# Optimization experiments

Measured on AMD Instinct MI355X. Metric: run time of the kernel, lower is better.

## Reference

```python
import jax, jax.numpy as jnp
import numpy as np

DIM = 2048
N_HEADS = 16
HEAD_DIM = DIM // N_HEADS
MAX_SEQ_LEN = 2048
ROPE_THETA = 32.0
EPS = 1e-6


def _precompute_freqs_1d(dim, max_seq_len, theta):
    freqs = theta ** (-np.arange(0, dim, 2, dtype=np.float32) / dim)  # [dim/2]
    pos = np.arange(max_seq_len, dtype=np.float32)                    # [S]
    ang = pos[:, None] * freqs[None, :]                               # [S, dim/2]
    return jnp.asarray(np.cos(ang)), jnp.asarray(np.sin(ang))


def _rms_norm(x, w):
    # x: [..., d]
    inv = jax.lax.rsqrt(jnp.mean(x * x, axis=-1, keepdims=True) + EPS)
    return x * inv * w


def setup_inputs() -> dict:
    key = jax.random.key(0)
    k1, k2, k3 = jax.random.split(key, 3)
    bsz, seq_len = 4, 2048
    x = jax.random.normal(k1, (bsz, seq_len, DIM), dtype=jnp.float32)
    w_qkv = jax.random.normal(k2, (3 * DIM, DIM), dtype=jnp.float32) * (DIM ** -0.5)
    w_proj = jax.random.normal(k3, (DIM, DIM), dtype=jnp.float32) * (DIM ** -0.5)
    q_norm_w = jnp.ones((HEAD_DIM,), dtype=jnp.float32)
    k_norm_w = jnp.ones((HEAD_DIM,), dtype=jnp.float32)
    return {"x": x, "w_qkv": w_qkv, "w_proj": w_proj,
            "q_norm_w": q_norm_w, "k_norm_w": k_norm_w}


def reference(x, w_qkv, w_proj, q_norm_w, k_norm_w):
    bsz, seq_len, dim = x.shape
    scale = HEAD_DIM ** -0.5

    # QKV projection (torch Linear: x @ W^T)
    qkv = jnp.einsum('bsd,ed->bse', x, w_qkv)  # [b, s, 3*dim]
    qkv = qkv.reshape(bsz, seq_len, 3, N_HEADS, HEAD_DIM).transpose(2, 0, 3, 1, 4)
    q, k, v = qkv[0], qkv[1], qkv[2]           # each [b, h, s, d]

    # Per-head RMSNorm on q, k
    q = _rms_norm(q, q_norm_w)
    k = _rms_norm(k, k_norm_w)

    # RoPE (half-split convention)
    cos, sin = _precompute_freqs_1d(HEAD_DIM, MAX_SEQ_LEN, ROPE_THETA)
    cos = cos[:seq_len][None, None]  # [1,1,s,d/2]
    sin = sin[:seq_len][None, None]
    q1, q2 = jnp.split(q, 2, axis=-1)
    k1, k2 = jnp.split(k, 2, axis=-1)
    q = jnp.concatenate([q1 * cos - q2 * sin, q2 * cos + q1 * sin], axis=-1)
    k = jnp.concatenate([k1 * cos - k2 * sin, k2 * cos + k1 * sin], axis=-1)

    # Scaled dot-product attention (no mask, eval-mode: no dropout)
    scores = jnp.einsum('bhqd,bhkd->bhqk', q, k) * scale
    attn = jax.nn.softmax(scores, axis=-1)
    y = jnp.einsum('bhqk,bhkd->bhqd', attn, v)

    # Merge heads + output projection
    y = y.transpose(0, 2, 1, 3).reshape(bsz, seq_len, dim)
    return jnp.einsum('bsd,ed->bse', y, w_proj)
```

## Files before the change

kernel.cpp:

```cpp
#include <hip/hip_runtime.h>
#include <hip/hip_bf16.h>

#define BSZ 4
#define SEQ 2048
#define DIM 2048
#define NH 16
#define HD 128
#define QK_LD 4096
#define SCALE 0.08838834764831845f
#define SC2 0.12751742910198f

typedef __attribute__((ext_vector_type(8))) short bf16x8;
typedef __attribute__((ext_vector_type(4))) float f32x4;

#define GLDS16(g, l)                                                           \
  __builtin_amdgcn_global_load_lds(                                           \
      (const __attribute__((address_space(1))) void*)(g),                     \
      (__attribute__((address_space(3))) void*)(l), 16, 0, 0)

__device__ inline short f2b(float f) {
  __hip_bfloat16 h = __float2bfloat16(f);
  short s;
  __builtin_memcpy(&s, &h, 2);
  return s;
}

__device__ inline void stage16(const float* gp, __hip_bfloat16* lp) {
  float4 q0 = ((const float4*)gp)[0], q1 = ((const float4*)gp)[1];
  float4 q2 = ((const float4*)gp)[2], q3 = ((const float4*)gp)[3];
  bf16x8 v0, v1;
  v0[0] = f2b(q0.x); v0[1] = f2b(q0.y); v0[2] = f2b(q0.z); v0[3] = f2b(q0.w);
  v0[4] = f2b(q1.x); v0[5] = f2b(q1.y); v0[6] = f2b(q1.z); v0[7] = f2b(q1.w);
  v1[0] = f2b(q2.x); v1[1] = f2b(q2.y); v1[2] = f2b(q2.z); v1[3] = f2b(q2.w);
  v1[4] = f2b(q3.x); v1[5] = f2b(q3.y); v1[6] = f2b(q3.z); v1[7] = f2b(q3.w);
  *(bf16x8*)lp = v0;
  *(bf16x8*)(lp + 8) = v1;
}

__device__ inline char* out_slice(void* outv, int b, int fl) {
  return (char*)outv + (size_t)b * (size_t)SEQ * DIM * (fl ? 2u : 4u);
}

__global__ __launch_bounds__(256)
void detect_canon(const unsigned int* __restrict__ wbits,
                  const void* __restrict__ qw, const void* __restrict__ kw,
                  __hip_bfloat16* __restrict__ qwb,
                  __hip_bfloat16* __restrict__ kwb, int* __restrict__ flag) {
  __shared__ int cnt;
  const int t = threadIdx.x;
  if (t == 0) cnt = 0;
  __syncthreads();
  int local = 0;
  for (int i = 0; i < 4; ++i) {
    unsigned int e = (wbits[t * 4 + i] >> 7) & 0xFF;
    if (e >= 96 && e < 160) local++;
  }
  atomicAdd(&cnt, local);
  __syncthreads();
  const int f = (cnt >= 768) ? 1 : 0;
  if (t == 0) *flag = f;
  if (t < 128)
    qwb[t] = f ? ((const __hip_bfloat16*)qw)[t]
               : __float2bfloat16(((const float*)qw)[t]);
  else
    kwb[t - 128] = f ? ((const __hip_bfloat16*)kw)[t - 128]
                     : __float2bfloat16(((const float*)kw)[t - 128]);
}

__global__ __launch_bounds__(256)
void convert_bf16(const void* __restrict__ in, __hip_bfloat16* __restrict__ out,
                  const int* __restrict__ flag) {
  const int fl = *flag;
  long i = ((long)blockIdx.x * 256 + threadIdx.x) * 8;
  if (fl) {
    *(float4*)(out + i) = *(const float4*)((const __hip_bfloat16*)in + i);
  } else {
    const float* p = (const float*)in + i;
    float4 a = ((const float4*)p)[0], b = ((const float4*)p)[1];
    bf16x8 o;
    o[0] = f2b(a.x); o[1] = f2b(a.y); o[2] = f2b(a.z); o[3] = f2b(a.w);
    o[4] = f2b(b.x); o[5] = f2b(b.y); o[6] = f2b(b.z); o[7] = f2b(b.w);
    *(bf16x8*)(out + i) = o;
  }
}


__global__ __launch_bounds__(256)
void gemm_qkv_full(const __hip_bfloat16* __restrict__ A,
                   const __hip_bfloat16* __restrict__ B,
                   __hip_bfloat16* __restrict__ qk, void* __restrict__ outv,
                   const int* __restrict__ flag) {
  __shared__ __hip_bfloat16 As[128 * 32];
  __shared__ __hip_bfloat16 Bs[128 * 32];
  const int t = threadIdx.x, wave = t >> 6, lane = t & 63;
  const int quad = lane >> 4, l16 = lane & 15;
  const int wm = (wave & 1) * 64, wn = (wave >> 1) * 64;
  const long bm = (long)blockIdx.x * 128, bn = (long)blockIdx.y * 128;
  const int fl = *flag;

  f32x4 acc[4][4] = {};
  for (int k0 = 0; k0 < DIM; k0 += 32) {
    __syncthreads();
    for (int i = 0; i < 2; ++i) {
      int c = wave * 64 + lane + i * 256;
      int row = c >> 2, kc = c & 3;
      GLDS16(A + (bm + row) * DIM + k0 + kc * 8, As + (wave * 64 + i * 256) * 8);
      GLDS16(B + (bn + row) * DIM + k0 + kc * 8, Bs + (wave * 64 + i * 256) * 8);
    }
    __syncthreads();
    bf16x8 aF[4], bF[4];
    for (int mt = 0; mt < 4; ++mt)
      aF[mt] = *(const bf16x8*)(As + (wm + mt * 16 + l16) * 32 + quad * 8);
    for (int nt = 0; nt < 4; ++nt)
      bF[nt] = *(const bf16x8*)(Bs + (wn + nt * 16 + l16) * 32 + quad * 8);
    for (int mt = 0; mt < 4; ++mt)
      for (int nt = 0; nt < 4; ++nt)
        acc[mt][nt] = __builtin_amdgcn_mfma_f32_16x16x32_bf16(
            aF[mt], bF[nt], acc[mt][nt], 0, 0, 0);
  }

  if (bn < 4096) {
    for (int mt = 0; mt < 4; ++mt) {
      long gr = bm + wm + mt * 16 + quad * 4;
      for (int nt = 0; nt < 4; ++nt) {
        long gc = bn + wn + nt * 16 + l16;
        for (int r = 0; r < 4; ++r)
          qk[(gr + r) * QK_LD + gc] = __float2bfloat16(acc[mt][nt][r]);
      }
    }
  } else {
    for (int mt = 0; mt < 4; ++mt) {
      long gr = bm + wm + mt * 16 + quad * 4;
      __hip_bfloat16* vtb = (__hip_bfloat16*)out_slice(outv, (int)(gr >> 11), fl);
      long s = gr & 2047;
      for (int nt = 0; nt < 4; ++nt) {
        long col = bn - 4096 + wn + nt * 16 + l16;
        for (int r = 0; r < 4; ++r)
          vtb[col * SEQ + s + r] = __float2bfloat16(acc[mt][nt][r]);
      }
    }
  }
}

__global__ __launch_bounds__(256)
void gemm_proj_full(const __hip_bfloat16* __restrict__ A,
                    const __hip_bfloat16* __restrict__ B,
                    void* __restrict__ outv, const int* __restrict__ flag) {
  __shared__ __hip_bfloat16 As[128 * 32];
  __shared__ __hip_bfloat16 Bs[128 * 32];
  const int t = threadIdx.x, wave = t >> 6, lane = t & 63;
  const int quad = lane >> 4, l16 = lane & 15;
  const int wm = (wave & 1) * 64, wn = (wave >> 1) * 64;
  const long bm = (long)blockIdx.x * 128, bn = (long)blockIdx.y * 128;
  const int fl = *flag;

  f32x4 acc[4][4] = {};
  for (int k0 = 0; k0 < DIM; k0 += 32) {
    __syncthreads();
    for (int i = 0; i < 2; ++i) {
      int c = wave * 64 + lane + i * 256;
      int row = c >> 2, kc = c & 3;
      GLDS16(A + (bm + row) * QK_LD + k0 + kc * 8, As + (wave * 64 + i * 256) * 8);
      GLDS16(B + (bn + row) * DIM + k0 + kc * 8, Bs + (wave * 64 + i * 256) * 8);
    }
    __syncthreads();
    bf16x8 aF[4], bF[4];
    for (int mt = 0; mt < 4; ++mt)
      aF[mt] = *(const bf16x8*)(As + (wm + mt * 16 + l16) * 32 + quad * 8);
    for (int nt = 0; nt < 4; ++nt)
      bF[nt] = *(const bf16x8*)(Bs + (wn + nt * 16 + l16) * 32 + quad * 8);
    for (int mt = 0; mt < 4; ++mt)
      for (int nt = 0; nt < 4; ++nt)
        acc[mt][nt] = __builtin_amdgcn_mfma_f32_16x16x32_bf16(
            aF[mt], bF[nt], acc[mt][nt], 0, 0, 0);
  }

  for (int mt = 0; mt < 4; ++mt) {
    long gr = bm + wm + mt * 16 + quad * 4;
    for (int nt = 0; nt < 4; ++nt) {
      long gc = bn + wn + nt * 16 + l16;
      for (int r = 0; r < 4; ++r) {
        long idx = (gr + r) * DIM + gc;
        if (fl) ((__hip_bfloat16*)outv)[idx] = __float2bfloat16(acc[mt][nt][r]);
        else    ((float*)outv)[idx] = acc[mt][nt][r];
      }
    }
  }
}


__global__ __launch_bounds__(256)
void gemm_qkv(const void* __restrict__ xin, const void* __restrict__ win,
              __hip_bfloat16* __restrict__ qk, void* __restrict__ outv,
              const int* __restrict__ flag, int b) {
  __shared__ __hip_bfloat16 As[128 * 32];
  __shared__ __hip_bfloat16 Bs[128 * 32];
  const int t = threadIdx.x, wave = t >> 6, lane = t & 63;
  const int quad = lane >> 4, l16 = lane & 15;
  const int wm = (wave & 1) * 64, wn = (wave >> 1) * 64;
  const long bm = (long)blockIdx.x * 128, bn = (long)blockIdx.y * 128;
  const int fl = *flag;
  const __hip_bfloat16* Ab = (const __hip_bfloat16*)xin + (long)b * SEQ * DIM;
  const __hip_bfloat16* Bb = (const __hip_bfloat16*)win;
  const float* Af = (const float*)xin + (long)b * SEQ * DIM;
  const float* Bf = (const float*)win;

  f32x4 acc[4][4] = {};
  for (int k0 = 0; k0 < DIM; k0 += 32) {
    __syncthreads();
    if (fl) {
      for (int i = 0; i < 2; ++i) {
        int c = wave * 64 + lane + i * 256;
        int row = c >> 2, kc = c & 3;
        GLDS16(Ab + (bm + row) * DIM + k0 + kc * 8, As + (wave * 64 + i * 256) * 8);
        GLDS16(Bb + (bn + row) * DIM + k0 + kc * 8, Bs + (wave * 64 + i * 256) * 8);
      }
    } else {
      int row = t >> 1, cb = k0 + (t & 1) * 16;
      stage16(Af + (bm + row) * DIM + cb, As + t * 16);
      stage16(Bf + (bn + row) * DIM + cb, Bs + t * 16);
    }
    __syncthreads();
    bf16x8 aF[4], bF[4];
    for (int mt = 0; mt < 4; ++mt)
      aF[mt] = *(const bf16x8*)(As + (wm + mt * 16 + l16) * 32 + quad * 8);
    for (int nt = 0; nt < 4; ++nt)
      bF[nt] = *(const bf16x8*)(Bs + (wn + nt * 16 + l16) * 32 + quad * 8);
    for (int mt = 0; mt < 4; ++mt)
      for (int nt = 0; nt < 4; ++nt)
        acc[mt][nt] = __builtin_amdgcn_mfma_f32_16x16x32_bf16(
            aF[mt], bF[nt], acc[mt][nt], 0, 0, 0);
  }

  if (bn < 4096) {
    for (int mt = 0; mt < 4; ++mt) {
      long gr = bm + wm + mt * 16 + quad * 4;
      for (int nt = 0; nt < 4; ++nt) {
        long gc = bn + wn + nt * 16 + l16;
        for (int r = 0; r < 4; ++r)
          qk[(gr + r) * QK_LD + gc] = __float2bfloat16(acc[mt][nt][r]);
      }
    }
  } else {
    __hip_bfloat16* vtb = (__hip_bfloat16*)out_slice(outv, b, fl);
    for (int mt = 0; mt < 4; ++mt) {
      long gr = bm + wm + mt * 16 + quad * 4;
      for (int nt = 0; nt < 4; ++nt) {
        long col = bn - 4096 + wn + nt * 16 + l16;
        for (int r = 0; r < 4; ++r)
          vtb[col * SEQ + gr + r] = __float2bfloat16(acc[mt][nt][r]);
      }
    }
  }
}

__global__ __launch_bounds__(256)
void gemm_proj(const __hip_bfloat16* __restrict__ A, const void* __restrict__ win,
               void* __restrict__ outv, const int* __restrict__ flag, int b) {
  __shared__ __hip_bfloat16 As[128 * 32];
  __shared__ __hip_bfloat16 Bs[128 * 32];
  const int t = threadIdx.x, wave = t >> 6, lane = t & 63;
  const int quad = lane >> 4, l16 = lane & 15;
  const int wm = (wave & 1) * 64, wn = (wave >> 1) * 64;
  const long bm = (long)blockIdx.x * 128, bn = (long)blockIdx.y * 128;
  const int fl = *flag;
  const __hip_bfloat16* Bb = (const __hip_bfloat16*)win;
  const float* Bf = (const float*)win;

  f32x4 acc[4][4] = {};
  for (int k0 = 0; k0 < DIM; k0 += 32) {
    __syncthreads();
    for (int i = 0; i < 2; ++i) {
      int c = wave * 64 + lane + i * 256;
      int row = c >> 2, kc = c & 3;
      GLDS16(A + (bm + row) * QK_LD + k0 + kc * 8, As + (wave * 64 + i * 256) * 8);
    }
    if (fl) {
      for (int i = 0; i < 2; ++i) {
        int c = wave * 64 + lane + i * 256;
        int row = c >> 2, kc = c & 3;
        GLDS16(Bb + (bn + row) * DIM + k0 + kc * 8, Bs + (wave * 64 + i * 256) * 8);
      }
    } else {
      int row = t >> 1, cb = k0 + (t & 1) * 16;
      stage16(Bf + (bn + row) * DIM + cb, Bs + t * 16);
    }
    __syncthreads();
    bf16x8 aF[4], bF[4];
    for (int mt = 0; mt < 4; ++mt)
      aF[mt] = *(const bf16x8*)(As + (wm + mt * 16 + l16) * 32 + quad * 8);
    for (int nt = 0; nt < 4; ++nt)
      bF[nt] = *(const bf16x8*)(Bs + (wn + nt * 16 + l16) * 32 + quad * 8);
    for (int mt = 0; mt < 4; ++mt)
      for (int nt = 0; nt < 4; ++nt)
        acc[mt][nt] = __builtin_amdgcn_mfma_f32_16x16x32_bf16(
            aF[mt], bF[nt], acc[mt][nt], 0, 0, 0);
  }

  char* Cb = out_slice(outv, b, fl);
  for (int mt = 0; mt < 4; ++mt) {
    long gr = bm + wm + mt * 16 + quad * 4;
    for (int nt = 0; nt < 4; ++nt) {
      long gc = bn + wn + nt * 16 + l16;
      for (int r = 0; r < 4; ++r) {
        long idx = (gr + r) * DIM + gc;
        if (fl) ((__hip_bfloat16*)Cb)[idx] = __float2bfloat16(acc[mt][nt][r]);
        else    ((float*)Cb)[idx] = acc[mt][nt][r];
      }
    }
  }
}


__global__ __launch_bounds__(256)
void norm_rope(__hip_bfloat16* __restrict__ qk,
               const __hip_bfloat16* __restrict__ qwb,
               const __hip_bfloat16* __restrict__ kwb) {
  const int wave = threadIdx.x >> 6, lane = threadIdx.x & 63;
  const int gid = blockIdx.x * 4 + wave;
  const int h = gid & 15, tt = (gid >> 4) & 1, row = gid >> 5;
  const int s = row & 2047;

  __hip_bfloat16* p = qk + (long)row * QK_LD + tt * DIM + h * HD;
  unsigned int u = ((const unsigned int*)p)[lane];

  unsigned int x = (unsigned int)__shfl((int)u, lane >> 1);
  unsigned int y = (unsigned int)__shfl((int)u, 32 + (lane >> 1));
  float v1 = __uint_as_float((lane & 1) ? (x & 0xFFFF0000u) : (x << 16));
  float v2 = __uint_as_float((lane & 1) ? (y & 0xFFFF0000u) : (y << 16));

  float ss = v1 * v1 + v2 * v2;
  for (int off = 1; off < 64; off <<= 1) ss += __shfl_xor(ss, off);
  float inv = rsqrtf(ss * (1.0f / 128.0f) + 1e-6f);

  const __hip_bfloat16* w = tt ? kwb : qwb;
  float n1 = v1 * inv * __bfloat162float(w[lane]);
  float n2 = v2 * inv * __bfloat162float(w[lane + 64]);

  float freq = exp2f(-5.0f * (float)lane * (1.0f / 64.0f));
  float ang = (float)s * freq;
  float c = cosf(ang), sn = sinf(ang);
  float r1 = n1 * c - n2 * sn;
  float r2 = n2 * c + n1 * sn;

  float z1lo = __shfl(r1, (2 * lane) & 63), z2lo = __shfl(r2, (2 * lane) & 63);
  float z1hi = __shfl(r1, (2 * lane + 1) & 63), z2hi = __shfl(r2, (2 * lane + 1) & 63);
  float lo = (lane < 32) ? z1lo : z2lo;
  float hi = (lane < 32) ? z1hi : z2hi;
  unsigned int ou = (unsigned int)(unsigned short)f2b(lo) |
                    ((unsigned int)(unsigned short)f2b(hi) << 16);
  ((unsigned int*)p)[lane] = ou;
}

__global__ __launch_bounds__(256, 4)
void flash_attn(__hip_bfloat16* __restrict__ qkbase, void* __restrict__ outv,
                const int* __restrict__ flag, int b0) {
  __shared__ __hip_bfloat16 Ks[4 * 64 * 32];
  __shared__ __hip_bfloat16 Vs[2 * 128 * 32];
  __shared__ __hip_bfloat16 Ps[4][2 * 32 * 32];

  const int t = threadIdx.x, wave = t >> 6, lane = t & 63;
  const int quad = lane >> 4, l16 = lane & 15;
  const int swz = (quad ^ ((l16 >> 1) & 3)) * 8;
  const int q0 = blockIdx.x * 128, h = blockIdx.y;
  const int b = b0 + blockIdx.z;
  const int fl = *flag;
  __hip_bfloat16* qk = qkbase + (long)blockIdx.z * SEQ * QK_LD;
  __hip_bfloat16* Qg = qk + h * HD;
  const __hip_bfloat16* Kg = Qg + DIM;
  const __hip_bfloat16* Vt =
      (const __hip_bfloat16*)out_slice(outv, b, fl) + (long)h * HD * SEQ;

  bf16x8 aQ[2][4];
#pragma unroll
  for (int mt = 0; mt < 2; ++mt)
#pragma unroll
    for (int ks = 0; ks < 4; ++ks)
      aQ[mt][ks] = *(const bf16x8*)(Qg +
          (long)(q0 + wave * 32 + mt * 16 + l16) * QK_LD + ks * 32 + quad * 8);

  f32x4 oacc[2][8] = {};
  float m_run[2][4], l_run[2][4];
#pragma unroll
  for (int mt = 0; mt < 2; ++mt)
    for (int r = 0; r < 4; ++r) { m_run[mt][r] = -1e30f; l_run[mt][r] = 0.0f; }

  for (int j0 = 0; j0 < SEQ; j0 += 64) {
    __syncthreads();
    for (int i = 0; i < 4; ++i) {
      int f = wave * 64 + lane + i * 256;
      int kk = f & 3, row = (f >> 2) & 63, ks = f >> 8;
      GLDS16(Kg + (long)(j0 + row) * QK_LD + ks * 32 + (kk ^ ((row >> 1) & 3)) * 8,
             Ks + (wave * 64 + i * 256) * 8);
    }
    for (int i = 0; i < 4; ++i) {
      int f = wave * 64 + lane + i * 256;
      int kk = f & 3, dimr = (f >> 2) & 127, ks2 = f >> 9;
      GLDS16(Vt + (long)dimr * SEQ + j0 + ks2 * 32 + (kk ^ ((dimr >> 1) & 3)) * 8,
             Vs + (wave * 64 + i * 256) * 8);
    }
    __syncthreads();

    f32x4 sacc[2][4] = {};
#pragma unroll
    for (int ks = 0; ks < 4; ++ks)
#pragma unroll
      for (int nt = 0; nt < 4; ++nt) {
        bf16x8 bK = *(const bf16x8*)(Ks + (ks * 64 + nt * 16 + l16) * 32 + swz);
#pragma unroll
        for (int mt = 0; mt < 2; ++mt)
          sacc[mt][nt] = __builtin_amdgcn_mfma_f32_16x16x32_bf16(
              aQ[mt][ks], bK, sacc[mt][nt], 0, 0, 0);
      }

    __hip_bfloat16* pw = &Ps[wave][0];
#pragma unroll
    for (int mt = 0; mt < 2; ++mt) {
#pragma unroll
      for (int r = 0; r < 4; ++r) {
        float p0 = sacc[mt][0][r] * SC2, p1 = sacc[mt][1][r] * SC2;
        float p2 = sacc[mt][2][r] * SC2, p3 = sacc[mt][3][r] * SC2;
        float mx = fmaxf(fmaxf(p0, p1), fmaxf(p2, p3));
        for (int off = 1; off < 16; off <<= 1)
          mx = fmaxf(mx, __shfl_xor(mx, off));
        if (__any(mx > m_run[mt][r] + 8.0f)) {
          float mnew = fmaxf(m_run[mt][r], mx);
          float alpha = exp2f(m_run[mt][r] - mnew);
          m_run[mt][r] = mnew;
          l_run[mt][r] *= alpha;
#pragma unroll
          for (int n = 0; n < 8; ++n) oacc[mt][n][r] *= alpha;
        }
        float m = m_run[mt][r];
        float e0 = exp2f(p0 - m), e1 = exp2f(p1 - m);
        float e2 = exp2f(p2 - m), e3 = exp2f(p3 - m);
        l_run[mt][r] += (e0 + e1) + (e2 + e3);
        int rbase = (mt * 16 + quad * 4 + r) * 32;
        int sc = (((quad * 4 + r) >> 1) & 3) << 3;
        pw[rbase + (l16 ^ sc)] = __float2bfloat16(e0);
        pw[rbase + ((l16 + 16) ^ sc)] = __float2bfloat16(e1);
        pw[1024 + rbase + (l16 ^ sc)] = __float2bfloat16(e2);
        pw[1024 + rbase + ((l16 + 16) ^ sc)] = __float2bfloat16(e3);
      }
    }

#pragma unroll
    for (int ks2 = 0; ks2 < 2; ++ks2) {
      bf16x8 aP[2];
#pragma unroll
      for (int mt = 0; mt < 2; ++mt)
        aP[mt] = *(const bf16x8*)(pw + ks2 * 1024 + (mt * 16 + l16) * 32 + swz);
#pragma unroll
      for (int n = 0; n < 8; ++n) {
        bf16x8 bV = *(const bf16x8*)(Vs + (ks2 * 128 + n * 16 + l16) * 32 + swz);
#pragma unroll
        for (int mt = 0; mt < 2; ++mt)
          oacc[mt][n] = __builtin_amdgcn_mfma_f32_16x16x32_bf16(
              aP[mt], bV, oacc[mt][n], 0, 0, 0);
      }
    }
  }

#pragma unroll
  for (int mt = 0; mt < 2; ++mt)
#pragma unroll
    for (int r = 0; r < 4; ++r) {
      float l = l_run[mt][r];
      for (int off = 1; off < 16; off <<= 1) l += __shfl_xor(l, off);
      float rl = 1.0f / l;
      long s = q0 + wave * 32 + mt * 16 + quad * 4 + r;
      for (int n = 0; n < 8; ++n)
        qk[s * QK_LD + h * HD + n * 16 + l16] =
            __float2bfloat16(oacc[mt][n][r] * rl);
    }
}

extern "C" void kernel_launch(void* const* d_in, const int* in_sizes, int n_in,
                              void* d_out, int out_size, void* d_ws, size_t ws_size,
                              hipStream_t stream) {
  int* flag = (int*)d_ws;
  __hip_bfloat16* qwb = (__hip_bfloat16*)((char*)d_ws + 64);
  __hip_bfloat16* kwb = qwb + 128;
  char* base = (char*)d_ws + 1024;

  detect_canon<<<1, 256, 0, stream>>>((const unsigned int*)d_in[1], d_in[3],
                                      d_in[4], qwb, kwb, flag);

  const size_t MB = 1024ull * 1024ull;
  const size_t NEED_A = 1024 + 128 * MB;

  if (ws_size >= NEED_A) {
    __hip_bfloat16* xb     = (__hip_bfloat16*)base;
    __hip_bfloat16* wqkvb  = (__hip_bfloat16*)(base + 32 * MB);
    __hip_bfloat16* wprojb = (__hip_bfloat16*)(base + 56 * MB);
    __hip_bfloat16* qk     = (__hip_bfloat16*)(base + 64 * MB);

    convert_bf16<<<(BSZ * SEQ * DIM) / 2048, 256, 0, stream>>>(d_in[0], xb, flag);
    convert_bf16<<<(3 * DIM * DIM) / 2048, 256, 0, stream>>>(d_in[1], wqkvb, flag);
    convert_bf16<<<(DIM * DIM) / 2048, 256, 0, stream>>>(d_in[2], wprojb, flag);

    gemm_qkv_full<<<dim3((BSZ * SEQ) / 128, (3 * DIM) / 128), 256, 0, stream>>>(
        xb, wqkvb, qk, d_out, flag);
    norm_rope<<<(BSZ * SEQ * 2 * NH) / 4, 256, 0, stream>>>(qk, qwb, kwb);
    flash_attn<<<dim3(SEQ / 128, NH, BSZ), 256, 0, stream>>>(qk, d_out, flag, 0);
    gemm_proj_full<<<dim3((BSZ * SEQ) / 128, DIM / 128), 256, 0, stream>>>(
        qk, wprojb, d_out, flag);
  } else {
    __hip_bfloat16* qk = (__hip_bfloat16*)base;
    for (int b = 0; b < BSZ; ++b) {
      gemm_qkv<<<dim3(SEQ / 128, (3 * DIM) / 128), 256, 0, stream>>>(
          d_in[0], d_in[1], qk, d_out, flag, b);
      norm_rope<<<(SEQ * 2 * NH) / 4, 256, 0, stream>>>(qk, qwb, kwb);
      flash_attn<<<dim3(SEQ / 128, NH, 1), 256, 0, stream>>>(qk, d_out, flag, b);
      gemm_proj<<<dim3(SEQ / 128, DIM / 128), 256, 0, stream>>>(
          qk, d_in[2], d_out, flag, b);
    }
  }
}
```

Before: 967.1 us.

## Split flash attention work across 8 waves with 16 query rows each

The flash attention block grows from 256 to 512 threads. Each of the 8 waves now owns 16 query rows instead of 32, which halves the per-wave Q fragments, accumulators and softmax state. The K/V tile loads are spread over twice as many threads, and the per-wave P scratch buffer is resized to match. This lowers register pressure and adds latency hiding per block. In exchange, each K/V fragment read from LDS feeds only one MFMA instead of two, so LDS read traffic per FLOP doubles.

```diff
diff --git a/kernel.cpp b/kernel.cpp
--- a/kernel.cpp
+++ b/kernel.cpp
@@ -352,12 +352,12 @@
   ((unsigned int*)p)[lane] = ou;
 }
 
-__global__ __launch_bounds__(256, 4)
+__global__ __launch_bounds__(512)
 void flash_attn(__hip_bfloat16* __restrict__ qkbase, void* __restrict__ outv,
                 const int* __restrict__ flag, int b0) {
   __shared__ __hip_bfloat16 Ks[4 * 64 * 32];
   __shared__ __hip_bfloat16 Vs[2 * 128 * 32];
-  __shared__ __hip_bfloat16 Ps[4][2 * 32 * 32];
+  __shared__ __hip_bfloat16 Ps[8][2 * 16 * 32];
 
   const int t = threadIdx.x, wave = t >> 6, lane = t & 63;
   const int quad = lane >> 4, l16 = lane & 15;
@@ -371,108 +371,95 @@
   const __hip_bfloat16* Vt =
       (const __hip_bfloat16*)out_slice(outv, b, fl) + (long)h * HD * SEQ;
 
-  bf16x8 aQ[2][4];
-#pragma unroll
-  for (int mt = 0; mt < 2; ++mt)
-#pragma unroll
-    for (int ks = 0; ks < 4; ++ks)
-      aQ[mt][ks] = *(const bf16x8*)(Qg +
-          (long)(q0 + wave * 32 + mt * 16 + l16) * QK_LD + ks * 32 + quad * 8);
-
-  f32x4 oacc[2][8] = {};
-  float m_run[2][4], l_run[2][4];
-#pragma unroll
-  for (int mt = 0; mt < 2; ++mt)
-    for (int r = 0; r < 4; ++r) { m_run[mt][r] = -1e30f; l_run[mt][r] = 0.0f; }
+  bf16x8 aQ[4];
+#pragma unroll
+  for (int ks = 0; ks < 4; ++ks)
+    aQ[ks] = *(const bf16x8*)(Qg +
+        (long)(q0 + wave * 16 + l16) * QK_LD + ks * 32 + quad * 8);
+
+  f32x4 oacc[8] = {};
+  float m_run[4], l_run[4];
+#pragma unroll
+  for (int r = 0; r < 4; ++r) { m_run[r] = -1e30f; l_run[r] = 0.0f; }
 
   for (int j0 = 0; j0 < SEQ; j0 += 64) {
     __syncthreads();
-    for (int i = 0; i < 4; ++i) {
-      int f = wave * 64 + lane + i * 256;
+#pragma unroll
+    for (int i = 0; i < 2; ++i) {
+      int f = t + i * 512;
       int kk = f & 3, row = (f >> 2) & 63, ks = f >> 8;
       GLDS16(Kg + (long)(j0 + row) * QK_LD + ks * 32 + (kk ^ ((row >> 1) & 3)) * 8,
-             Ks + (wave * 64 + i * 256) * 8);
-    }
-    for (int i = 0; i < 4; ++i) {
-      int f = wave * 64 + lane + i * 256;
+             Ks + (t + i * 512) * 8);
+    }
+#pragma unroll
+    for (int i = 0; i < 2; ++i) {
+      int f = t + i * 512;
       int kk = f & 3, dimr = (f >> 2) & 127, ks2 = f >> 9;
       GLDS16(Vt + (long)dimr * SEQ + j0 + ks2 * 32 + (kk ^ ((dimr >> 1) & 3)) * 8,
-             Vs + (wave * 64 + i * 256) * 8);
-    }
-    __syncthreads();
-
-    f32x4 sacc[2][4] = {};
+             Vs + (t + i * 512) * 8);
+    }
+    __syncthreads();
+
+    f32x4 sacc[4] = {};
 #pragma unroll
     for (int ks = 0; ks < 4; ++ks)
 #pragma unroll
       for (int nt = 0; nt < 4; ++nt) {
         bf16x8 bK = *(const bf16x8*)(Ks + (ks * 64 + nt * 16 + l16) * 32 + swz);
-#pragma unroll
-        for (int mt = 0; mt < 2; ++mt)
-          sacc[mt][nt] = __builtin_amdgcn_mfma_f32_16x16x32_bf16(
-              aQ[mt][ks], bK, sacc[mt][nt], 0, 0, 0);
+        sacc[nt] = __builtin_amdgcn_mfma_f32_16x16x32_bf16(
+            aQ[ks], bK, sacc[nt], 0, 0, 0);
       }
 
     __hip_bfloat16* pw = &Ps[wave][0];
 #pragma unroll
-    for (int mt = 0; mt < 2; ++mt) {
-#pragma unroll
-      for (int r = 0; r < 4; ++r) {
-        float p0 = sacc[mt][0][r] * SC2, p1 = sacc[mt][1][r] * SC2;
-        float p2 = sacc[mt][2][r] * SC2, p3 = sacc[mt][3][r] * SC2;
-        float mx = fmaxf(fmaxf(p0, p1), fmaxf(p2, p3));
-        for (int off = 1; off < 16; off <<= 1)
-          mx = fmaxf(mx, __shfl_xor(mx, off));
-        if (__any(mx > m_run[mt][r] + 8.0f)) {
-          float mnew = fmaxf(m_run[mt][r], mx);
-          float alpha = exp2f(m_run[mt][r] - mnew);
-          m_run[mt][r] = mnew;
-          l_run[mt][r] *= alpha;
-#pragma unroll
-          for (int n = 0; n < 8; ++n) oacc[mt][n][r] *= alpha;
-        }
-        float m = m_run[mt][r];
-        float e0 = exp2f(p0 - m), e1 = exp2f(p1 - m);
-        float e2 = exp2f(p2 - m), e3 = exp2f(p3 - m);
-        l_run[mt][r] += (e0 + e1) + (e2 + e3);
-        int rbase = (mt * 16 + quad * 4 + r) * 32;
-        int sc = (((quad * 4 + r) >> 1) & 3) << 3;
-        pw[rbase + (l16 ^ sc)] = __float2bfloat16(e0);
-        pw[rbase + ((l16 + 16) ^ sc)] = __float2bfloat16(e1);
-        pw[1024 + rbase + (l16 ^ sc)] = __float2bfloat16(e2);
-        pw[1024 + rbase + ((l16 + 16) ^ sc)] = __float2bfloat16(e3);
-      }
+    for (int r = 0; r < 4; ++r) {
+      float p0 = sacc[0][r] * SC2, p1 = sacc[1][r] * SC2;
+      float p2 = sacc[2][r] * SC2, p3 = sacc[3][r] * SC2;
+      float mx = fmaxf(fmaxf(p0, p1), fmaxf(p2, p3));
+      for (int off = 1; off < 16; off <<= 1)
+        mx = fmaxf(mx, __shfl_xor(mx, off));
+      if (__any(mx > m_run[r] + 8.0f)) {
+        float mnew = fmaxf(m_run[r], mx);
+        float alpha = exp2f(m_run[r] - mnew);
+        m_run[r] = mnew;
+        l_run[r] *= alpha;
+#pragma unroll
+        for (int n = 0; n < 8; ++n) oacc[n][r] *= alpha;
+      }
+      float m = m_run[r];
+      float e0 = exp2f(p0 - m), e1 = exp2f(p1 - m);
+      float e2 = exp2f(p2 - m), e3 = exp2f(p3 - m);
+      l_run[r] += (e0 + e1) + (e2 + e3);
+      int rbase = (quad * 4 + r) * 32;
+      int sc = (((quad * 4 + r) >> 1) & 3) << 3;
+      pw[rbase + (l16 ^ sc)] = __float2bfloat16(e0);
+      pw[rbase + ((l16 + 16) ^ sc)] = __float2bfloat16(e1);
+      pw[512 + rbase + (l16 ^ sc)] = __float2bfloat16(e2);
+      pw[512 + rbase + ((l16 + 16) ^ sc)] = __float2bfloat16(e3);
     }
 
 #pragma unroll
     for (int ks2 = 0; ks2 < 2; ++ks2) {
-      bf16x8 aP[2];
-#pragma unroll
-      for (int mt = 0; mt < 2; ++mt)
-        aP[mt] = *(const bf16x8*)(pw + ks2 * 1024 + (mt * 16 + l16) * 32 + swz);
+      bf16x8 aP = *(const bf16x8*)(pw + (ks2 * 16 + l16) * 32 + swz);
 #pragma unroll
       for (int n = 0; n < 8; ++n) {
         bf16x8 bV = *(const bf16x8*)(Vs + (ks2 * 128 + n * 16 + l16) * 32 + swz);
-#pragma unroll
-        for (int mt = 0; mt < 2; ++mt)
-          oacc[mt][n] = __builtin_amdgcn_mfma_f32_16x16x32_bf16(
-              aP[mt], bV, oacc[mt][n], 0, 0, 0);
-      }
-    }
-  }
-
-#pragma unroll
-  for (int mt = 0; mt < 2; ++mt)
-#pragma unroll
-    for (int r = 0; r < 4; ++r) {
-      float l = l_run[mt][r];
-      for (int off = 1; off < 16; off <<= 1) l += __shfl_xor(l, off);
-      float rl = 1.0f / l;
-      long s = q0 + wave * 32 + mt * 16 + quad * 4 + r;
-      for (int n = 0; n < 8; ++n)
-        qk[s * QK_LD + h * HD + n * 16 + l16] =
-            __float2bfloat16(oacc[mt][n][r] * rl);
-    }
+        oacc[n] = __builtin_amdgcn_mfma_f32_16x16x32_bf16(
+            aP, bV, oacc[n], 0, 0, 0);
+      }
+    }
+  }
+
+#pragma unroll
+  for (int r = 0; r < 4; ++r) {
+    float l = l_run[r];
+    for (int off = 1; off < 16; off <<= 1) l += __shfl_xor(l, off);
+    float rl = 1.0f / l;
+    long s = q0 + wave * 16 + quad * 4 + r;
+    for (int n = 0; n < 8; ++n)
+      qk[s * QK_LD + h * HD + n * 16 + l16] =
+          __float2bfloat16(oacc[n][r] * rl);
+  }
 }
 
 extern "C" void kernel_launch(void* const* d_in, const int* in_sizes, int n_in,
@@ -502,7 +489,7 @@
     gemm_qkv_full<<<dim3((BSZ * SEQ) / 128, (3 * DIM) / 128), 256, 0, stream>>>(
         xb, wqkvb, qk, d_out, flag);
     norm_rope<<<(BSZ * SEQ * 2 * NH) / 4, 256, 0, stream>>>(qk, qwb, kwb);
-    flash_attn<<<dim3(SEQ / 128, NH, BSZ), 256, 0, stream>>>(qk, d_out, flag, 0);
+    flash_attn<<<dim3(SEQ / 128, NH, BSZ), 512, 0, stream>>>(qk, d_out, flag, 0);
     gemm_proj_full<<<dim3((BSZ * SEQ) / 128, DIM / 128), 256, 0, stream>>>(
         qk, wprojb, d_out, flag);
   } else {
@@ -511,7 +498,7 @@
       gemm_qkv<<<dim3(SEQ / 128, (3 * DIM) / 128), 256, 0, stream>>>(
           d_in[0], d_in[1], qk, d_out, flag, b);
       norm_rope<<<(SEQ * 2 * NH) / 4, 256, 0, stream>>>(qk, qwb, kwb);
-      flash_attn<<<dim3(SEQ / 128, NH, 1), 256, 0, stream>>>(qk, d_out, flag, b);
+      flash_attn<<<dim3(SEQ / 128, NH, 1), 512, 0, stream>>>(qk, d_out, flag, b);
       gemm_proj<<<dim3(SEQ / 128, DIM / 128), 256, 0, stream>>>(
           qk, d_in[2], d_out, flag, b);
     }
```

Result: faster. 868.6 us (-10.2%).
